# Kernel tuning notes

Measured on AMD Instinct MI355X. Metric: run time of the kernel, lower is better.

The kernel has to match this reference:

```python
import jax, jax.numpy as jnp
import numpy as np

B, S, D, H = 4, 4096, 512, 2
PD = D // H  # projection_dim = 256


def setup_inputs() -> dict:
    key = jax.random.key(0)
    ks = jax.random.split(key, 6)
    scale = 1.0 / np.sqrt(D)
    return {
        "x": jax.random.normal(ks[0], (B, S, D), dtype=jnp.float32),
        "Wq": jax.random.normal(ks[1], (D, D), dtype=jnp.float32) * scale,
        "bq": jnp.zeros((D,), dtype=jnp.float32),
        "Wk": jax.random.normal(ks[2], (D, D), dtype=jnp.float32) * scale,
        "bk": jnp.zeros((D,), dtype=jnp.float32),
        "Wv": jax.random.normal(ks[3], (D, D), dtype=jnp.float32) * scale,
        "bv": jnp.zeros((D,), dtype=jnp.float32),
        "Wo": jax.random.normal(ks[4], (D, D), dtype=jnp.float32) * scale,
        "bo": jnp.zeros((D,), dtype=jnp.float32),
    }


def _split_heads(t):
    # [B, S, D] -> [B, H, S, PD]
    return t.reshape(B, S, H, PD).transpose(0, 2, 1, 3)


def reference(x, Wq, bq, Wk, bk, Wv, bv, Wo, bo):
    Q = _split_heads(x @ Wq + bq)
    K = _split_heads(x @ Wk + bk)
    V = _split_heads(x @ Wv + bv)
    # scaled dot-product attention, non-causal (no mask in original)
    scores = jnp.einsum("bhqd,bhkd->bhqk", Q, K) / jnp.sqrt(jnp.float32(PD))
    weights = jax.nn.softmax(scores, axis=-1)
    attn = jnp.einsum("bhqk,bhkd->bhqd", weights, V)
    # merge heads: [B, H, S, PD] -> [B, S, D]
    concat = attn.transpose(0, 2, 1, 3).reshape(B, S, D)
    return concat @ Wo + bo
```

## Files before the change

kernel.cpp:

```cpp
#include <hip/hip_runtime.h>
#include <hip/hip_bf16.h>


#define B_  4
#define S_  4096
#define D_  512
#define H_  2
#define PD_ 256
#define SC2 0.09016844f

typedef __attribute__((ext_vector_type(4))) float f32x4;
typedef __attribute__((ext_vector_type(16))) float f32x16;
typedef __attribute__((ext_vector_type(8))) short short8;
typedef __attribute__((ext_vector_type(4))) short short4v;
typedef __attribute__((ext_vector_type(4))) unsigned u32x4;

static __device__ __forceinline__ short f2bf(float f) {
  unsigned u = __float_as_uint(f);
  u += 0x7fffu + ((u >> 16) & 1u);
  return (short)(u >> 16);
}
static __device__ __forceinline__ unsigned pack2(float a, float b) {
  return (unsigned)(unsigned short)f2bf(a) | ((unsigned)(unsigned short)f2bf(b) << 16);
}
static __device__ __forceinline__ void gload16(const short* g, short* l) {
  __builtin_amdgcn_global_load_lds((const __attribute__((address_space(1))) void*)g,
                                   (__attribute__((address_space(3))) void*)l,
                                   16, 0, 0);
}

__global__ void convert_x_kernel(const float* __restrict__ x, short* __restrict__ xb, int n8) {
  int i = blockIdx.x * blockDim.x + threadIdx.x;
  int stride = gridDim.x * blockDim.x;
  for (; i < n8; i += stride) {
    const f32x4* p = (const f32x4*)(x + (size_t)i * 8);
    f32x4 a = p[0], b = p[1];
    short8 v;
    v[0] = f2bf(a[0]); v[1] = f2bf(a[1]); v[2] = f2bf(a[2]); v[3] = f2bf(a[3]);
    v[4] = f2bf(b[0]); v[5] = f2bf(b[1]); v[6] = f2bf(b[2]); v[7] = f2bf(b[3]);
    *(short8*)(xb + (size_t)i * 8) = v;
  }
}

__global__ __launch_bounds__(256) void transpose_w(
    const float* __restrict__ W0, const float* __restrict__ W1,
    const float* __restrict__ W2, const float* __restrict__ W3,
    short* __restrict__ T0, short* __restrict__ T1,
    short* __restrict__ T2, short* __restrict__ T3) {
  const float* W = (blockIdx.z == 0) ? W0 : (blockIdx.z == 1) ? W1 : (blockIdx.z == 2) ? W2 : W3;
  short* T = (blockIdx.z == 0) ? T0 : (blockIdx.z == 1) ? T1 : (blockIdx.z == 2) ? T2 : T3;
  __shared__ float tile[32][33];
  int tx = threadIdx.x & 31, ty = threadIdx.x >> 5;
  int r0 = blockIdx.x * 32, c0 = blockIdx.y * 32;
#pragma unroll
  for (int i = 0; i < 4; ++i)
    tile[ty + 8 * i][tx] = W[(size_t)(r0 + ty + 8 * i) * D_ + c0 + tx];
  __syncthreads();
#pragma unroll
  for (int i = 0; i < 4; ++i)
    T[(size_t)(c0 + ty + 8 * i) * D_ + r0 + tx] = f2bf(tile[tx][ty + 8 * i]);
}

__global__ __launch_bounds__(256) void transpose_v(
    const short* __restrict__ Vw, short* __restrict__ Vt) {
  __shared__ short tile[64][68];
  int h = blockIdx.z;
  int s0 = blockIdx.x * 64, d0 = blockIdx.y * 64;
  const short* src = Vw + (size_t)h * S_ * PD_;
  short* dst = Vt + (size_t)h * S_ * PD_;
  int tx = threadIdx.x & 15, ty = threadIdx.x >> 4;
#pragma unroll
  for (int i = 0; i < 4; ++i) {
    short4v v = *(const short4v*)(src + (size_t)(s0 + ty + 16 * i) * PD_ + d0 + tx * 4);
    *(short4v*)&tile[ty + 16 * i][tx * 4] = v;
  }
  __syncthreads();
#pragma unroll
  for (int i = 0; i < 4; ++i) {
    int d = d0 + ty + 16 * i;
    short4v v;
#pragma unroll
    for (int j = 0; j < 4; ++j) v[j] = tile[tx * 4 + j][ty + 16 * i];
    int swz = ((tx >> 1) & 3) ^ ((d >> 1) & 3);
    *(short4v*)(dst + (size_t)d * S_ + s0 + (tx >> 3) * 32 + swz * 8 + (tx & 1) * 4) = v;
  }
}

template <int MODE>
__global__ __launch_bounds__(256, 2) void gemm_bt(
    const short* __restrict__ A,
    const short* __restrict__ Bt0, const short* __restrict__ Bt1, const short* __restrict__ Bt2,
    const float* __restrict__ b0, const float* __restrict__ b1, const float* __restrict__ b2,
    short* __restrict__ o0, short* __restrict__ o1, short* __restrict__ o2,
    float* __restrict__ fout) {
  __shared__ short sA[128 * 72];
  __shared__ short sB[128 * 72];

  const int tid = threadIdx.x;
  const int lane = tid & 63, wid = tid >> 6;
  const int wr = wid >> 1, wc = wid & 1;
  const int l15 = lane & 15, g = lane >> 4;
  const int m0 = blockIdx.x * 128, n0 = blockIdx.y * 128;

  const short* Bt = (MODE == 0) ? ((blockIdx.z == 0) ? Bt0 : (blockIdx.z == 1) ? Bt1 : Bt2) : Bt0;
  const float* bias = (MODE == 0) ? ((blockIdx.z == 0) ? b0 : (blockIdx.z == 1) ? b1 : b2) : b0;

  short8 pa[4], pb[4];

  auto loadT = [&](int kt) {
#pragma unroll
    for (int i = 0; i < 4; ++i) {
      int slot = tid + 256 * i;
      int r = slot >> 3, gg = slot & 7;
      pa[i] = *(const short8*)(A + (size_t)(m0 + r) * D_ + kt * 64 + 8 * gg);
      pb[i] = *(const short8*)(Bt + (size_t)(n0 + r) * D_ + kt * 64 + 8 * gg);
    }
  };
  auto storeT = [&]() {
#pragma unroll
    for (int i = 0; i < 4; ++i) {
      int slot = tid + 256 * i;
      int r = slot >> 3, gg = slot & 7;
      *(short8*)&sA[r * 72 + 8 * gg] = pa[i];
      *(short8*)&sB[r * 72 + 8 * gg] = pb[i];
    }
  };

  f32x4 acc[4][4];
#pragma unroll
  for (int i = 0; i < 4; ++i)
#pragma unroll
    for (int j = 0; j < 4; ++j) acc[i][j] = (f32x4)0.0f;

  loadT(0);
#pragma unroll 1
  for (int kt = 0; kt < 8; ++kt) {
    __syncthreads();
    storeT();
    if (kt < 7) loadT(kt + 1);
    __syncthreads();
#pragma unroll
    for (int s = 0; s < 2; ++s) {
      short8 a[4], b[4];
#pragma unroll
      for (int fr = 0; fr < 4; ++fr)
        a[fr] = *(const short8*)&sA[(wr * 64 + fr * 16 + l15) * 72 + 32 * s + 8 * g];
#pragma unroll
      for (int fc = 0; fc < 4; ++fc)
        b[fc] = *(const short8*)&sB[(wc * 64 + fc * 16 + l15) * 72 + 32 * s + 8 * g];
#pragma unroll
      for (int fr = 0; fr < 4; ++fr)
#pragma unroll
        for (int fc = 0; fc < 4; ++fc)
          acc[fr][fc] = __builtin_amdgcn_mfma_f32_16x16x32_bf16(a[fr], b[fc], acc[fr][fc], 0, 0, 0);
    }
  }

  if (MODE == 0) {
    short* dst = (blockIdx.z == 0) ? o0 : (blockIdx.z == 1) ? o1 : o2;
    const bool kswz = (blockIdx.z == 1);
#pragma unroll
    for (int fc = 0; fc < 4; ++fc) {
      int n = n0 + wc * 64 + fc * 16 + l15;
      float bvv = bias[n];
      int h = n >> 8, pd = n & 255;
#pragma unroll
      for (int fr = 0; fr < 4; ++fr)
#pragma unroll
        for (int r = 0; r < 4; ++r) {
          int m = m0 + wr * 64 + fr * 16 + 4 * g + r;
          int bb = m >> 12, ss = m & 4095;
          int pdw = pd;
          if (kswz) {
            int ch = pd >> 3;
            pdw = (pd & 7) | (((ch & 24) | ((ch & 7) ^ (ss & 7))) << 3);
          }
          dst[((size_t)((bb * H_ + h) * S_ + ss)) * PD_ + pdw] = f2bf(acc[fr][fc][r] + bvv);
        }
    }
  } else {
#pragma unroll
    for (int fc = 0; fc < 4; ++fc) {
      int n = n0 + wc * 64 + fc * 16 + l15;
      float bvv = bias[n];
#pragma unroll
      for (int fr = 0; fr < 4; ++fr)
#pragma unroll
        for (int r = 0; r < 4; ++r) {
          int m = m0 + wr * 64 + fr * 16 + 4 * g + r;
          fout[(size_t)m * D_ + n] = acc[fr][fc][r] + bvv;
        }
    }
  }
}

__global__ __launch_bounds__(256, 2) void attn3_kernel(
    const short* __restrict__ Qw, const short* __restrict__ Kw,
    const short* __restrict__ Vt, short* __restrict__ ATT) {
  __shared__ __align__(16) char smem[66560];
  __shared__ float sB1[4][32];
  __shared__ float sMm[4][32];
  __shared__ float sMl[2][32];
  short* sK0 = (short*)smem;
  short* sK1 = (short*)(smem + 16384);
  short* sV0 = (short*)(smem + 32768);
  short* sV1 = (short*)(smem + 49152);

  const int tid = threadIdx.x, lane = tid & 63, w = tid >> 6;
  const int l31 = lane & 31, hi = lane >> 5;
  const int head = blockIdx.x & 7, qb = blockIdx.x >> 3;
  const size_t hoff = (size_t)head * S_ * PD_;
  const short* Qh = Qw + hoff;
  const short* Kh = Kw + hoff;
  const short* Vh = Vt + hoff;
  const int wbase = tid & ~63;
  const int kh = w >> 1;
  const int kbase = kh * 2048;

  short* sKh = kh ? sK1 : sK0;
  short* sVh = kh ? sV1 : sV0;

  const int qrow = qb * 64 + (w & 1) * 32 + l31;
  short8 qf[16];
#pragma unroll
  for (int dc = 0; dc < 16; ++dc)
    qf[dc] = *(const short8*)(Qh + (size_t)qrow * PD_ + dc * 16 + hi * 8);

  f32x16 o[8];
#pragma unroll
  for (int i = 0; i < 8; ++i) o[i] = (f32x16)0.0f;
  float mrun = -3.0e38f, lrun = 0.0f;

  auto stage = [&](int t) {
    const int k0 = t * 32;
#pragma unroll
    for (int i = 0; i < 4; ++i) {
      int s = tid + 256 * i;
      short* ldst = (short*)((char*)nullptr);
      (void)ldst;
      gload16(Kh + (size_t)(k0 + (s >> 5)) * PD_ + (s & 31) * 8,
              sK0 + (size_t)(wbase + 256 * i) * 8);
      gload16(Kh + (size_t)(2048 + k0 + (s >> 5)) * PD_ + (s & 31) * 8,
              sK1 + (size_t)(wbase + 256 * i) * 8);
      gload16(Vh + (size_t)(s >> 2) * S_ + k0 + (s & 3) * 8,
              sV0 + (size_t)(wbase + 256 * i) * 8);
      gload16(Vh + (size_t)(s >> 2) * S_ + 2048 + k0 + (s & 3) * 8,
              sV1 + (size_t)(wbase + 256 * i) * 8);
    }
  };

#pragma unroll 1
  for (int t = 0; t < 64; ++t) {
    __syncthreads();
    stage(t);
    __syncthreads();

    f32x16 sacc = (f32x16)0.0f;
#pragma unroll
    for (int dc = 0; dc < 16; ++dc) {
      int ch = (2 * dc + hi) ^ (l31 & 7);
      short8 kf = *(const short8*)&sKh[l31 * 256 + ch * 8];
      sacc = __builtin_amdgcn_mfma_f32_32x32x16_bf16(kf, qf[dc], sacc, 0, 0, 0);
    }

    float tmax = sacc[0];
#pragma unroll
    for (int r = 1; r < 16; ++r) tmax = fmaxf(tmax, sacc[r]);
    tmax = fmaxf(tmax, __shfl_xor(tmax, 32));
    if (!__all(tmax <= mrun + 16.0f)) {
      float mn = fmaxf(mrun, tmax);
      float resc = exp2f((mrun - mn) * SC2);
      mrun = mn;
      lrun *= resc;
      if (!hi) sB1[w][l31] = resc;
      asm volatile("" ::: "memory");
      f32x4 rv0 = *(const f32x4*)&sB1[w][0 + hi * 4];
      f32x4 rv1 = *(const f32x4*)&sB1[w][8 + hi * 4];
      f32x4 rv2 = *(const f32x4*)&sB1[w][16 + hi * 4];
      f32x4 rv3 = *(const f32x4*)&sB1[w][24 + hi * 4];
#pragma unroll
      for (int dcb = 0; dcb < 8; ++dcb)
#pragma unroll
        for (int r = 0; r < 16; ++r) {
          float rr = (r < 4 ? rv0 : r < 8 ? rv1 : r < 12 ? rv2 : rv3)[r & 3];
          o[dcb][r] *= rr;
        }
    }
    float lsum = 0.0f;
#pragma unroll
    for (int r = 0; r < 16; ++r) {
      float p = exp2f((sacc[r] - mrun) * SC2);
      sacc[r] = p;
      lsum += p;
    }
    lsum += __shfl_xor(lsum, 32);
    lrun += lsum;

#pragma unroll
    for (int c = 0; c < 2; ++c) {
      unsigned pk0 = pack2(sacc[8 * c + 0], sacc[8 * c + 1]);
      unsigned pk1 = pack2(sacc[8 * c + 2], sacc[8 * c + 3]);
      unsigned pk2 = pack2(sacc[8 * c + 4], sacc[8 * c + 5]);
      unsigned pk3 = pack2(sacc[8 * c + 6], sacc[8 * c + 7]);
      unsigned sh0 = __shfl_xor(pk0, 32);
      unsigned sh1 = __shfl_xor(pk1, 32);
      unsigned sh2 = __shfl_xor(pk2, 32);
      unsigned sh3 = __shfl_xor(pk3, 32);
      u32x4 ua;
      ua[0] = hi ? sh2 : pk0;
      ua[1] = hi ? sh3 : pk1;
      ua[2] = hi ? pk2 : sh0;
      ua[3] = hi ? pk3 : sh1;
      short8 af = *(short8*)&ua;
      const int ch = (2 * c + hi) ^ ((l31 >> 1) & 3);
#pragma unroll
      for (int dcb = 0; dcb < 8; ++dcb) {
        short8 vf = *(const short8*)&sVh[(size_t)(dcb * 32 + l31) * 32 + ch * 8];
        o[dcb] = __builtin_amdgcn_mfma_f32_32x32x16_bf16(af, vf, o[dcb], 0, 0, 0);
      }
    }
  }

  __syncthreads();
  if (!hi) sMm[w][l31] = mrun;
  __syncthreads();
  {
    float mo = sMm[w ^ 2][l31];
    float mf = fmaxf(mrun, mo);
    float sc = exp2f((mrun - mf) * SC2);
    lrun *= sc;
    if (!hi) sB1[w][l31] = sc;
    asm volatile("" ::: "memory");
    f32x4 rv0 = *(const f32x4*)&sB1[w][0 + hi * 4];
    f32x4 rv1 = *(const f32x4*)&sB1[w][8 + hi * 4];
    f32x4 rv2 = *(const f32x4*)&sB1[w][16 + hi * 4];
    f32x4 rv3 = *(const f32x4*)&sB1[w][24 + hi * 4];
#pragma unroll
    for (int dcb = 0; dcb < 8; ++dcb)
#pragma unroll
      for (int r = 0; r < 16; ++r) {
        float rr = (r < 4 ? rv0 : r < 8 ? rv1 : r < 12 ? rv2 : rv3)[r & 3];
        o[dcb][r] *= rr;
      }
    if (w >= 2 && !hi) sMl[w - 2][l31] = lrun;
  }
  __syncthreads();
  float* mb = (float*)smem;
  if (w >= 2) {
    float* rg = mb + (size_t)(w - 2) * 8320;
#pragma unroll
    for (int dcb = 0; dcb < 8; ++dcb)
#pragma unroll
      for (int r4 = 0; r4 < 4; ++r4) {
        f32x4 v;
        v[0] = o[dcb][4 * r4 + 0];
        v[1] = o[dcb][4 * r4 + 1];
        v[2] = o[dcb][4 * r4 + 2];
        v[3] = o[dcb][4 * r4 + 3];
        *(f32x4*)&rg[(size_t)(dcb * 4 + r4) * 260 + lane * 4] = v;
      }
  }
  __syncthreads();
  if (w < 2) {
    float* rg = mb + (size_t)w * 8320;
#pragma unroll
    for (int dcb = 0; dcb < 8; ++dcb)
#pragma unroll
      for (int r4 = 0; r4 < 4; ++r4) {
        f32x4 v = *(const f32x4*)&rg[(size_t)(dcb * 4 + r4) * 260 + lane * 4];
        o[dcb][4 * r4 + 0] += v[0];
        o[dcb][4 * r4 + 1] += v[1];
        o[dcb][4 * r4 + 2] += v[2];
        o[dcb][4 * r4 + 3] += v[3];
      }
    lrun += sMl[w][l31];
    if (!hi) sB1[w][l31] = 1.0f / lrun;
    asm volatile("" ::: "memory");
    f32x4 iv0 = *(const f32x4*)&sB1[w][0 + hi * 4];
    f32x4 iv1 = *(const f32x4*)&sB1[w][8 + hi * 4];
    f32x4 iv2 = *(const f32x4*)&sB1[w][16 + hi * 4];
    f32x4 iv3 = *(const f32x4*)&sB1[w][24 + hi * 4];
    const int bb = head >> 1, hh = head & 1;
#pragma unroll
    for (int r = 0; r < 16; ++r) {
      int q = qb * 64 + (w & 1) * 32 + (r & 3) + 8 * (r >> 2) + 4 * hi;
      float iv = (r < 4 ? iv0 : r < 8 ? iv1 : r < 12 ? iv2 : iv3)[r & 3];
      size_t base = ((size_t)(bb * S_ + q)) * D_ + hh * PD_;
#pragma unroll
      for (int dcb = 0; dcb < 8; ++dcb)
        ATT[base + dcb * 32 + l31] = f2bf(o[dcb][r] * iv);
    }
  }
}

extern "C" void kernel_launch(void* const* d_in, const int* in_sizes, int n_in,
                              void* d_out, int out_size, void* d_ws, size_t ws_size,
                              hipStream_t stream) {
  const float* x  = (const float*)d_in[0];
  const float* Wq = (const float*)d_in[1];
  const float* bq = (const float*)d_in[2];
  const float* Wk = (const float*)d_in[3];
  const float* bk = (const float*)d_in[4];
  const float* Wv = (const float*)d_in[5];
  const float* bv = (const float*)d_in[6];
  const float* Wo = (const float*)d_in[7];
  const float* bo = (const float*)d_in[8];
  float* out = (float*)d_out;

  char* ws = (char*)d_ws;
  const size_t WSZ = (size_t)D_ * D_ * 2;
  const size_t QSZ = (size_t)B_ * H_ * S_ * PD_ * 2;
  short* wtq = (short*)(ws);
  short* wtk = (short*)(ws + WSZ);
  short* wtv = (short*)(ws + 2 * WSZ);
  short* wto = (short*)(ws + 3 * WSZ);
  short* Qw  = (short*)(ws + 4 * WSZ);
  short* Kw  = (short*)(ws + 4 * WSZ + QSZ);
  short* Vw  = (short*)(ws + 4 * WSZ + 2 * QSZ);
  short* ATT = (short*)(ws + 4 * WSZ + 3 * QSZ);
  short* XB  = ATT;
  short* Vtp = (short*)d_out;

  convert_x_kernel<<<dim3(2048), dim3(256), 0, stream>>>(x, XB, (B_ * S_ * D_) / 8);
  transpose_w<<<dim3(16, 16, 4), dim3(256), 0, stream>>>(Wq, Wk, Wv, Wo, wtq, wtk, wtv, wto);
  gemm_bt<0><<<dim3(128, 4, 3), dim3(256), 0, stream>>>(
      XB, wtq, wtk, wtv, bq, bk, bv, Qw, Kw, Vw, (float*)nullptr);
  transpose_v<<<dim3(64, 4, 8), dim3(256), 0, stream>>>(Vw, Vtp);
  attn3_kernel<<<dim3(512), dim3(256), 0, stream>>>(Qw, Kw, Vtp, ATT);
  gemm_bt<1><<<dim3(128, 4, 1), dim3(256), 0, stream>>>(
      ATT, wto, wto, wto, bo, bo, bo, nullptr, nullptr, nullptr, out);
}
```

Baseline: 292.6 us.

## Double-buffer attention K/V tiles with 512-thread blocks and prescaled Q

The attention kernel is rewritten as 8 waves per block covering 128 query rows, with K/V tiles double-buffered in shared memory so the next tile's global-to-LDS load overlaps the current tile's compute. This drops one barrier pair per tile and halves how often each K/V tile is reloaded per query. The softmax scale is folded into Q in the projection GEMM epilogue, so the exp2 arguments no longer need a multiply. Bf16 packing uses the hardware v_cvt_pk_bf16_f32 instruction, and the K/V shared-memory swizzles change. In exchange the block uses about 130KB of LDS, which limits occupancy, and rounding Q to bf16 after scaling slightly changes numerics.

```diff
diff --git a/kernel.cpp b/kernel.cpp
--- a/kernel.cpp
+++ b/kernel.cpp
@@ -7,7 +7,7 @@
 #define D_  512
 #define H_  2
 #define PD_ 256
-#define SC2 0.09016844f
+#define QSCALE 0.09016844f
 
 typedef __attribute__((ext_vector_type(4))) float f32x4;
 typedef __attribute__((ext_vector_type(16))) float f32x16;
@@ -20,10 +20,12 @@
   u += 0x7fffu + ((u >> 16) & 1u);
   return (short)(u >> 16);
 }
-static __device__ __forceinline__ unsigned pack2(float a, float b) {
-  return (unsigned)(unsigned short)f2bf(a) | ((unsigned)(unsigned short)f2bf(b) << 16);
-}
-static __device__ __forceinline__ void gload16(const short* g, short* l) {
+static __device__ __forceinline__ unsigned cvtpk(float a, float b) {
+  unsigned r;
+  asm("v_cvt_pk_bf16_f32 %0, %1, %2" : "=v"(r) : "v"(a), "v"(b));
+  return r;
+}
+static __device__ __forceinline__ void gload16(const short* g, const short* l) {
   __builtin_amdgcn_global_load_lds((const __attribute__((address_space(1))) void*)g,
                                    (__attribute__((address_space(3))) void*)l,
                                    16, 0, 0);
@@ -81,7 +83,7 @@
     short4v v;
 #pragma unroll
     for (int j = 0; j < 4; ++j) v[j] = tile[tx * 4 + j][ty + 16 * i];
-    int swz = ((tx >> 1) & 3) ^ ((d >> 1) & 3);
+    int swz = ((tx >> 1) & 3) ^ ((d >> 3) & 3);
     *(short4v*)(dst + (size_t)d * S_ + s0 + (tx >> 3) * 32 + swz * 8 + (tx & 1) * 4) = v;
   }
 }
@@ -159,6 +161,7 @@
   if (MODE == 0) {
     short* dst = (blockIdx.z == 0) ? o0 : (blockIdx.z == 1) ? o1 : o2;
     const bool kswz = (blockIdx.z == 1);
+    const float sc = (blockIdx.z == 0) ? QSCALE : 1.0f;
 #pragma unroll
     for (int fc = 0; fc < 4; ++fc) {
       int n = n0 + wc * 64 + fc * 16 + l15;
@@ -175,7 +178,7 @@
             int ch = pd >> 3;
             pdw = (pd & 7) | (((ch & 24) | ((ch & 7) ^ (ss & 7))) << 3);
           }
-          dst[((size_t)((bb * H_ + h) * S_ + ss)) * PD_ + pdw] = f2bf(acc[fr][fc][r] + bvv);
+          dst[((size_t)((bb * H_ + h) * S_ + ss)) * PD_ + pdw] = f2bf((acc[fr][fc][r] + bvv) * sc);
         }
     }
   } else {
@@ -194,82 +197,84 @@
   }
 }
 
-__global__ __launch_bounds__(256, 2) void attn3_kernel(
+__global__ __launch_bounds__(512, 2) void attn4_kernel(
     const short* __restrict__ Qw, const short* __restrict__ Kw,
     const short* __restrict__ Vt, short* __restrict__ ATT) {
-  __shared__ __align__(16) char smem[66560];
-  __shared__ float sB1[4][32];
-  __shared__ float sMm[4][32];
-  __shared__ float sMl[2][32];
-  short* sK0 = (short*)smem;
-  short* sK1 = (short*)(smem + 16384);
-  short* sV0 = (short*)(smem + 32768);
-  short* sV1 = (short*)(smem + 49152);
+  __shared__ __align__(16) char smem[133120];
+  __shared__ float sMm[8][32];
+  __shared__ float sB1[8][32];
+  __shared__ float sMl[4][32];
 
   const int tid = threadIdx.x, lane = tid & 63, w = tid >> 6;
   const int l31 = lane & 31, hi = lane >> 5;
   const int head = blockIdx.x & 7, qb = blockIdx.x >> 3;
+  const int kh = w >> 2, qg = w & 3;
   const size_t hoff = (size_t)head * S_ * PD_;
   const short* Qh = Qw + hoff;
   const short* Kh = Kw + hoff;
   const short* Vh = Vt + hoff;
-  const int wbase = tid & ~63;
-  const int kh = w >> 1;
-  const int kbase = kh * 2048;
-
-  short* sKh = kh ? sK1 : sK0;
-  short* sVh = kh ? sV1 : sV0;
-
-  const int qrow = qb * 64 + (w & 1) * 32 + l31;
+
+  const int qrow = qb * 128 + qg * 32 + l31;
   short8 qf[16];
 #pragma unroll
   for (int dc = 0; dc < 16; ++dc)
     qf[dc] = *(const short8*)(Qh + (size_t)qrow * PD_ + dc * 16 + hi * 8);
 
+  const int mm = l31 & 7, pp = (l31 >> 1) & 3, q3 = l31 >> 3;
+  int kaddr[4];
+#pragma unroll
+  for (int b = 0; b < 4; ++b)
+    kaddr[b] = kh * 32768 + l31 * 512 + ((b ^ pp) << 5) + ((hi ^ (mm & 1)) << 4);
+  int vaddr[2];
+#pragma unroll
+  for (int c = 0; c < 2; ++c)
+    vaddr[c] = 65536 + kh * 32768 + l31 * 64 + (((2 * c + hi) ^ q3) << 4);
+
   f32x16 o[8];
 #pragma unroll
   for (int i = 0; i < 8; ++i) o[i] = (f32x16)0.0f;
   float mrun = -3.0e38f, lrun = 0.0f;
 
-  auto stage = [&](int t) {
-    const int k0 = t * 32;
+  auto stage = [&](int buf, int t) {
+    const short* kt = Kh + (size_t)(t * 32) * PD_;
 #pragma unroll
     for (int i = 0; i < 4; ++i) {
-      int s = tid + 256 * i;
-      short* ldst = (short*)((char*)nullptr);
-      (void)ldst;
-      gload16(Kh + (size_t)(k0 + (s >> 5)) * PD_ + (s & 31) * 8,
-              sK0 + (size_t)(wbase + 256 * i) * 8);
-      gload16(Kh + (size_t)(2048 + k0 + (s >> 5)) * PD_ + (s & 31) * 8,
-              sK1 + (size_t)(wbase + 256 * i) * 8);
-      gload16(Vh + (size_t)(s >> 2) * S_ + k0 + (s & 3) * 8,
-              sV0 + (size_t)(wbase + 256 * i) * 8);
-      gload16(Vh + (size_t)(s >> 2) * S_ + 2048 + k0 + (s & 3) * 8,
-              sV1 + (size_t)(wbase + 256 * i) * 8);
+      int s = tid + 512 * i;
+      int half = s >> 10, s1 = s & 1023;
+      gload16(kt + (size_t)(half * 2048) * PD_ + (s1 >> 5) * PD_ + (s1 & 31) * 8,
+              (const short*)(smem + half * 32768 + buf * 16384 + s1 * 16));
+    }
+    const short* vt = Vh + t * 32;
+#pragma unroll
+    for (int i = 0; i < 4; ++i) {
+      int s = tid + 512 * i;
+      int half = s >> 10, s1 = s & 1023;
+      gload16(vt + (size_t)(s1 >> 2) * S_ + half * 2048 + (s1 & 3) * 8,
+              (const short*)(smem + 65536 + half * 32768 + buf * 16384 + s1 * 16));
     }
   };
 
-#pragma unroll 1
-  for (int t = 0; t < 64; ++t) {
-    __syncthreads();
-    stage(t);
-    __syncthreads();
-
-    f32x16 sacc = (f32x16)0.0f;
-#pragma unroll
-    for (int dc = 0; dc < 16; ++dc) {
-      int ch = (2 * dc + hi) ^ (l31 & 7);
-      short8 kf = *(const short8*)&sKh[l31 * 256 + ch * 8];
-      sacc = __builtin_amdgcn_mfma_f32_32x32x16_bf16(kf, qf[dc], sacc, 0, 0, 0);
-    }
-
-    float tmax = sacc[0];
-#pragma unroll
-    for (int r = 1; r < 16; ++r) tmax = fmaxf(tmax, sacc[r]);
+  auto compute = [&](int buf) {
+    f32x16 sa = (f32x16)0.0f, sb = (f32x16)0.0f;
+#pragma unroll
+    for (int a = 0; a < 4; ++a)
+#pragma unroll
+      for (int b = 0; b < 4; ++b) {
+        short8 kf = *(const short8*)(smem + kaddr[b] + a * 128 + buf * 16384);
+        if (a < 2)
+          sa = __builtin_amdgcn_mfma_f32_32x32x16_bf16(kf, qf[4 * a + b], sa, 0, 0, 0);
+        else
+          sb = __builtin_amdgcn_mfma_f32_32x32x16_bf16(kf, qf[4 * a + b], sb, 0, 0, 0);
+      }
+    f32x16 sacc = sa + sb;
+
+    float tmax = fmaxf(sacc[0], sacc[1]);
+#pragma unroll
+    for (int r = 2; r < 16; ++r) tmax = fmaxf(tmax, sacc[r]);
     tmax = fmaxf(tmax, __shfl_xor(tmax, 32));
-    if (!__all(tmax <= mrun + 16.0f)) {
+    if (!__all(tmax <= mrun + 8.0f)) {
       float mn = fmaxf(mrun, tmax);
-      float resc = exp2f((mrun - mn) * SC2);
+      float resc = exp2f(mrun - mn);
       mrun = mn;
       lrun *= resc;
       if (!hi) sB1[w][l31] = resc;
@@ -289,19 +294,19 @@
     float lsum = 0.0f;
 #pragma unroll
     for (int r = 0; r < 16; ++r) {
-      float p = exp2f((sacc[r] - mrun) * SC2);
-      sacc[r] = p;
-      lsum += p;
+      float pv = exp2f(sacc[r] - mrun);
+      sacc[r] = pv;
+      lsum += pv;
     }
     lsum += __shfl_xor(lsum, 32);
     lrun += lsum;
 
 #pragma unroll
     for (int c = 0; c < 2; ++c) {
-      unsigned pk0 = pack2(sacc[8 * c + 0], sacc[8 * c + 1]);
-      unsigned pk1 = pack2(sacc[8 * c + 2], sacc[8 * c + 3]);
-      unsigned pk2 = pack2(sacc[8 * c + 4], sacc[8 * c + 5]);
-      unsigned pk3 = pack2(sacc[8 * c + 6], sacc[8 * c + 7]);
+      unsigned pk0 = cvtpk(sacc[8 * c + 0], sacc[8 * c + 1]);
+      unsigned pk1 = cvtpk(sacc[8 * c + 2], sacc[8 * c + 3]);
+      unsigned pk2 = cvtpk(sacc[8 * c + 4], sacc[8 * c + 5]);
+      unsigned pk3 = cvtpk(sacc[8 * c + 6], sacc[8 * c + 7]);
       unsigned sh0 = __shfl_xor(pk0, 32);
       unsigned sh1 = __shfl_xor(pk1, 32);
       unsigned sh2 = __shfl_xor(pk2, 32);
@@ -312,22 +317,32 @@
       ua[2] = hi ? pk2 : sh0;
       ua[3] = hi ? pk3 : sh1;
       short8 af = *(short8*)&ua;
-      const int ch = (2 * c + hi) ^ ((l31 >> 1) & 3);
 #pragma unroll
       for (int dcb = 0; dcb < 8; ++dcb) {
-        short8 vf = *(const short8*)&sVh[(size_t)(dcb * 32 + l31) * 32 + ch * 8];
+        short8 vf = *(const short8*)(smem + vaddr[c] + dcb * 2048 + buf * 16384);
         o[dcb] = __builtin_amdgcn_mfma_f32_32x32x16_bf16(af, vf, o[dcb], 0, 0, 0);
       }
     }
+  };
+
+  stage(0, 0);
+#pragma unroll 1
+  for (int t = 0; t < 64; t += 2) {
+    __syncthreads();
+    stage(1, t + 1);
+    compute(0);
+    __syncthreads();
+    if (t + 2 < 64) stage(0, t + 2);
+    compute(1);
   }
 
   __syncthreads();
   if (!hi) sMm[w][l31] = mrun;
   __syncthreads();
   {
-    float mo = sMm[w ^ 2][l31];
+    float mo = sMm[w ^ 4][l31];
     float mf = fmaxf(mrun, mo);
-    float sc = exp2f((mrun - mf) * SC2);
+    float sc = exp2f(mrun - mf);
     lrun *= sc;
     if (!hi) sB1[w][l31] = sc;
     asm volatile("" ::: "memory");
@@ -342,12 +357,12 @@
         float rr = (r < 4 ? rv0 : r < 8 ? rv1 : r < 12 ? rv2 : rv3)[r & 3];
         o[dcb][r] *= rr;
       }
-    if (w >= 2 && !hi) sMl[w - 2][l31] = lrun;
+    if (w >= 4 && !hi) sMl[w - 4][l31] = lrun;
   }
   __syncthreads();
   float* mb = (float*)smem;
-  if (w >= 2) {
-    float* rg = mb + (size_t)(w - 2) * 8320;
+  if (w >= 4) {
+    float* rg = mb + (size_t)qg * 8320;
 #pragma unroll
     for (int dcb = 0; dcb < 8; ++dcb)
 #pragma unroll
@@ -361,8 +376,8 @@
       }
   }
   __syncthreads();
-  if (w < 2) {
-    float* rg = mb + (size_t)w * 8320;
+  if (w < 4) {
+    float* rg = mb + (size_t)qg * 8320;
 #pragma unroll
     for (int dcb = 0; dcb < 8; ++dcb)
 #pragma unroll
@@ -373,7 +388,7 @@
         o[dcb][4 * r4 + 2] += v[2];
         o[dcb][4 * r4 + 3] += v[3];
       }
-    lrun += sMl[w][l31];
+    lrun += sMl[qg][l31];
     if (!hi) sB1[w][l31] = 1.0f / lrun;
     asm volatile("" ::: "memory");
     f32x4 iv0 = *(const f32x4*)&sB1[w][0 + hi * 4];
@@ -383,7 +398,7 @@
     const int bb = head >> 1, hh = head & 1;
 #pragma unroll
     for (int r = 0; r < 16; ++r) {
-      int q = qb * 64 + (w & 1) * 32 + (r & 3) + 8 * (r >> 2) + 4 * hi;
+      int q = qb * 128 + qg * 32 + (r & 3) + 8 * (r >> 2) + 4 * hi;
       float iv = (r < 4 ? iv0 : r < 8 ? iv1 : r < 12 ? iv2 : iv3)[r & 3];
       size_t base = ((size_t)(bb * S_ + q)) * D_ + hh * PD_;
 #pragma unroll
@@ -426,7 +441,7 @@
   gemm_bt<0><<<dim3(128, 4, 3), dim3(256), 0, stream>>>(
       XB, wtq, wtk, wtv, bq, bk, bv, Qw, Kw, Vw, (float*)nullptr);
   transpose_v<<<dim3(64, 4, 8), dim3(256), 0, stream>>>(Vw, Vtp);
-  attn3_kernel<<<dim3(512), dim3(256), 0, stream>>>(Qw, Kw, Vtp, ATT);
+  attn4_kernel<<<dim3(256), dim3(512), 0, stream>>>(Qw, Kw, Vtp, ATT);
   gemm_bt<1><<<dim3(128, 4, 1), dim3(256), 0, stream>>>(
       ATT, wto, wto, wto, bo, bo, bo, nullptr, nullptr, nullptr, out);
 }
```

Result: no change. 290.2 us (-0.8%).
